# Performance work log

Measured on AMD Instinct MI355X. Metric: run time of the kernel, lower is better.

Reference implementation:

```python
import jax, jax.numpy as jnp
import numpy as np

NUM_HEADS = 16


def setup_inputs() -> dict:
    key = jax.random.key(0)
    ks = jax.random.split(key, 8)
    B, L, Hd = 2, 2048, 1024
    s = 0.02
    return {
        "x": jax.random.normal(ks[0], (B, L, Hd), jnp.float32),
        "y": jax.random.normal(ks[1], (B, L, Hd), jnp.float32),
        "mask": jnp.zeros((B, L), jnp.bool_),  # True = padding (masked out)
        "Wq_w": jax.random.normal(ks[2], (Hd, Hd), jnp.float32) * s,
        "Wq_b": jnp.zeros((Hd,), jnp.float32),
        "Wkv_w": jax.random.normal(ks[3], (Hd, 2 * Hd), jnp.float32) * s,
        "Wkv_b": jnp.zeros((2 * Hd,), jnp.float32),
        "proj_w": jax.random.normal(ks[4], (Hd, Hd), jnp.float32) * s,
        "proj_b": jnp.zeros((Hd,), jnp.float32),
    }


def reference(x, y, mask, Wq_w, Wq_b, Wkv_w, Wkv_b, proj_w, proj_b):
    B, L, Hd = x.shape
    H = NUM_HEADS
    D = Hd // H
    scale = 1.0 / np.sqrt(D)

    # projections (torch Linear: stored here already as (in, out))
    q = (x @ Wq_w + Wq_b).reshape(B, L, H, D).transpose(0, 2, 1, 3)   # bhld
    kv = (y @ Wkv_w + Wkv_b).reshape(B, L, 2, H, D)
    k = kv[:, :, 0].transpose(0, 2, 1, 3)                             # bhkd
    v = kv[:, :, 1].transpose(0, 2, 1, 3)                             # bhkd

    attn = jnp.einsum("bhld,bhkd->bhlk", q, k) * scale

    # combined padding (over keys) + causal mask; True = masked
    causal = jnp.triu(jnp.ones((L, L), jnp.bool_), 1)                 # (L, L)
    combined = mask[:, None, None, :] | causal[None, None]            # (B,1,L,L)
    attn = jnp.where(combined, -jnp.inf, attn)

    p = jax.nn.softmax(attn, axis=-1)
    out = jnp.einsum("bhlk,bhkd->bhld", p, v)
    out = out.transpose(0, 2, 1, 3).reshape(B, L, Hd)
    return out @ proj_w + proj_b
```

## Files before the change

kernel.cpp:

```cpp
#include <hip/hip_runtime.h>
#include <stdint.h>

#define B_  2
#define L_  2048
#define HD_ 1024
#define H_  16
#define D_  64

typedef unsigned short u16;
typedef __attribute__((ext_vector_type(8))) short bf16x8;
typedef __attribute__((ext_vector_type(4))) float f32x4;

#define MFMA16(a, b, c) __builtin_amdgcn_mfma_f32_16x16x32_bf16((a), (b), (c), 0, 0, 0)

__device__ __forceinline__ void gload16(const void* g, void* l) {
  __builtin_amdgcn_global_load_lds((const __attribute__((address_space(1))) void*)g,
                                   (__attribute__((address_space(3))) void*)l, 16, 0, 0);
}

__device__ __forceinline__ u16 f2bf(float f) {
  union { float f; uint32_t u; } c; c.f = f;
  uint32_t u = c.u + 0x7FFFu + ((c.u >> 16) & 1u);
  return (u16)(u >> 16);
}

__device__ __forceinline__ uint32_t cvt_pk_bf16(float lo, float hi) {
  uint32_t r;
  asm("v_cvt_pk_bf16_f32 %0, %1, %2" : "=v"(r) : "v"(lo), "v"(hi));
  return r;
}

__global__ void cast2_k(const float* __restrict__ x, const float* __restrict__ y,
                        u16* __restrict__ xb, u16* __restrict__ yb) {
  int bid = blockIdx.x;
  const float* in = bid < 2048 ? x : y;
  u16* out = bid < 2048 ? xb : yb;
  int i = ((bid & 2047) * 256 + threadIdx.x) * 8;
  float4 a = *(const float4*)(in + i);
  float4 b = *(const float4*)(in + i + 4);
  bf16x8 r;
  r[0] = (short)f2bf(a.x); r[1] = (short)f2bf(a.y); r[2] = (short)f2bf(a.z); r[3] = (short)f2bf(a.w);
  r[4] = (short)f2bf(b.x); r[5] = (short)f2bf(b.y); r[6] = (short)f2bf(b.z); r[7] = (short)f2bf(b.w);
  *(bf16x8*)(out + i) = r;
}

__global__ void wtrans_k(const float* __restrict__ Wq, const float* __restrict__ Wkv,
                         const float* __restrict__ Wp,
                         u16* __restrict__ Wqt, u16* __restrict__ Wkvt, u16* __restrict__ Wpt) {
  int z = blockIdx.z;
  const float* src = z == 0 ? Wq : (z == 1 ? Wkv : Wp);
  u16* dst = z == 0 ? Wqt : (z == 1 ? Wkvt : Wpt);
  int Nfull = (z == 1) ? 2048 : 1024;
  int nb = blockIdx.x * 32;
  if (nb >= Nfull) return;
  __shared__ float tile[32][33];
  int t = threadIdx.x;
  int tc = t & 31, tr = t >> 5;
  int kb = blockIdx.y * 32;
#pragma unroll
  for (int i = 0; i < 4; i++)
    tile[tr + i * 8][tc] = src[(size_t)(kb + tr + i * 8) * Nfull + nb + tc];
  __syncthreads();
#pragma unroll
  for (int i = 0; i < 4; i++) {
    int nl = tr + i * 8;
    dst[(size_t)(nb + nl) * 1024 + kb + tc] = f2bf(tile[tc][nl]);
  }
}

__device__ __forceinline__ void gemm_body(
    char* sA, char* sB,
    const u16* __restrict__ A, const u16* __restrict__ Bt,
    const float* __restrict__ bias, void* __restrict__ outp,
    int N, int epi, int bm, int bn)
{
  int t = threadIdx.x;
  int lane = t & 63, w = t >> 6;
  int g = lane >> 4, l15 = lane & 15;
  int wr = w >> 1, wc = w & 1;

  f32x4 zero = {0.f, 0.f, 0.f, 0.f};
  f32x4 acc[4][4];
#pragma unroll
  for (int mi = 0; mi < 4; mi++)
#pragma unroll
    for (int ni = 0; ni < 4; ni++) acc[mi][ni] = zero;

#define GSTAGE(bufi, k0s) do {                                                          \
    _Pragma("unroll")                                                                   \
    for (int it = 0; it < 4; it++) {                                                    \
      int c = it * 256 + t;                          \
      int r = c >> 3, sp = c & 7;                                                       \
      int off = (sp ^ (r & 7)) << 4;               \
      gload16((const char*)(A + (size_t)(bm + r) * 1024 + (k0s)) + off,                 \
              sA + (bufi) * 16384 + c * 16);                                            \
      gload16((const char*)(Bt + (size_t)(bn + r) * 1024 + (k0s)) + off,                \
              sB + (bufi) * 16384 + c * 16);                                            \
    } } while (0)

  GSTAGE(0, 0);
  int buf = 0;
#pragma unroll 1
  for (int kt = 0; kt < 16; kt++) {
    __builtin_amdgcn_sched_barrier(0);
    __builtin_amdgcn_s_barrier();
    if (kt < 15) {
      GSTAGE(buf ^ 1, (kt + 1) << 6);
      asm volatile("s_waitcnt vmcnt(8)" ::: "memory");
    } else {
      asm volatile("s_waitcnt vmcnt(0)" ::: "memory");
    }
    __builtin_amdgcn_s_barrier();
    __builtin_amdgcn_sched_barrier(0);

    const char* cA = sA + buf * 16384;
    const char* cB = sB + buf * 16384;
#pragma unroll
    for (int kc = 0; kc < 2; kc++) {
      bf16x8 af[4], bfr[4];
#pragma unroll
      for (int mi = 0; mi < 4; mi++) {
        int r = wr * 64 + mi * 16 + l15;
        af[mi] = *(const bf16x8*)(cA + r * 128 + (((kc * 4 + g) ^ (r & 7)) << 4));
      }
#pragma unroll
      for (int ni = 0; ni < 4; ni++) {
        int r = wc * 64 + ni * 16 + l15;
        bfr[ni] = *(const bf16x8*)(cB + r * 128 + (((kc * 4 + g) ^ (r & 7)) << 4));
      }
#pragma unroll
      for (int mi = 0; mi < 4; mi++)
#pragma unroll
        for (int ni = 0; ni < 4; ni++)
          acc[mi][ni] = MFMA16(af[mi], bfr[ni], acc[mi][ni]);
    }
    buf ^= 1;
  }
#undef GSTAGE

  float bv[4];
#pragma unroll
  for (int ni = 0; ni < 4; ni++) bv[ni] = bias[bn + wc * 64 + ni * 16 + l15];

  if (epi == 2) {
    float* fo = (float*)outp;
#pragma unroll
    for (int mi = 0; mi < 4; mi++)
#pragma unroll
      for (int ni = 0; ni < 4; ni++) {
        int n = bn + wc * 64 + ni * 16 + l15;
#pragma unroll
        for (int r = 0; r < 4; r++) {
          int m = bm + wr * 64 + mi * 16 + g * 4 + r;
          fo[(size_t)m * N + n] = acc[mi][ni][r] + bv[ni];
        }
      }
  } else {
    u16* ob = (u16*)outp;
#pragma unroll
    for (int mi = 0; mi < 4; mi++)
#pragma unroll
      for (int ni = 0; ni < 4; ni++) {
        int n = bn + wc * 64 + ni * 16 + l15;
        int kv = n >> 10;
        int hh = (n >> 6) & 15;
        int dd = n & 63;
        int m0 = bm + wr * 64 + mi * 16 + g * 4;
        int bb = m0 >> 11, lq0 = m0 & 2047;
        if (epi == 1 && kv == 1) {
          ushort4 pk;
          pk.x = f2bf(acc[mi][ni][0] + bv[ni]);
          pk.y = f2bf(acc[mi][ni][1] + bv[ni]);
          pk.z = f2bf(acc[mi][ni][2] + bv[ni]);
          pk.w = f2bf(acc[mi][ni][3] + bv[ni]);
          size_t idx = (size_t)(B_ * H_ * L_ * D_) +
                       (((size_t)(bb * H_ + hh) * D_ + dd) * L_ + lq0);
          *(ushort4*)(ob + idx) = pk;
        } else {
#pragma unroll
          for (int r = 0; r < 4; r++) {
            size_t idx = (((size_t)(bb * H_ + hh) * L_ + lq0 + r) * D_) + dd;
            ob[idx] = f2bf(acc[mi][ni][r] + bv[ni]);
          }
        }
      }
  }
}

__global__ __launch_bounds__(256) void qkv_k(
    const u16* __restrict__ xb, const u16* __restrict__ yb,
    const u16* __restrict__ Wqt, const u16* __restrict__ Wkvt,
    const float* __restrict__ Wq_b, const float* __restrict__ Wkv_b,
    u16* __restrict__ Qout, u16* __restrict__ KVout)
{
  __shared__ char sA[2 * 16384];
  __shared__ char sB[2 * 16384];
  int bx = blockIdx.x, by = blockIdx.y;
  if (by < 16) {
    gemm_body(sA, sB, yb, Wkvt, Wkv_b, (void*)KVout, 2048, 1, by * 128, bx * 128);
    __syncthreads();
    gemm_body(sA, sB, yb, Wkvt, Wkv_b, (void*)KVout, 2048, 1, (by + 16) * 128, bx * 128);
  } else {
    gemm_body(sA, sB, xb, Wqt, Wq_b, (void*)Qout, 1024, 0,
              (2 * (by - 16) + (bx >> 3)) * 128, (bx & 7) * 128);
  }
}

__global__ __launch_bounds__(256) void gemm_k(
    const u16* __restrict__ A, const u16* __restrict__ Bt,
    const float* __restrict__ bias, void* __restrict__ outp, int N)
{
  __shared__ char sA[2 * 16384];
  __shared__ char sB[2 * 16384];
  gemm_body(sA, sB, A, Bt, bias, outp, N, 2, blockIdx.y * 128, blockIdx.x * 128);
}

__global__ __launch_bounds__(512, 2) void attn_k(
    const u16* __restrict__ Qb, const u16* __restrict__ Kb, const u16* __restrict__ Vt,
    const unsigned char* __restrict__ pad, u16* __restrict__ Ob)
{
  __shared__ char sK[3][8192];
  __shared__ char sV[3][8192];
  __shared__ char sP[8][2048];
  int t = threadIdx.x, lane = t & 63, w = t >> 6, g = lane >> 4, l15 = lane & 15;
  int x = blockIdx.x, h = blockIdx.y, b = blockIdx.z, bh = b * H_ + h;
  int qb = b ? x : 15 - x;

  const u16* Kbh = Kb + (size_t)bh * L_ * D_;
  const u16* Vbh = Vt + (size_t)bh * D_ * L_;
  const unsigned char* pdb = pad + b * L_;
  const float SCL = 0.125f * 1.44269504089f;
  int psw = l15 & 7;

  int srr = t >> 3, ssp = t & 7;
  int sso = (ssp ^ (srr & 7)) << 4;
#define STAGE(bufi, kt0s) do {                                                        \
    gload16((const char*)(Kbh + (size_t)((kt0s) + srr) * D_) + sso, sK[bufi] + t * 16); \
    gload16((const char*)(Vbh + (size_t)srr * L_ + (kt0s)) + sso, sV[bufi] + t * 16);   \
  } while (0)

  int qw0 = qb * 128 + w * 16;
  int bound = qw0 + 15;
  int nkt = 2 * qb + 2;

  const u16* qp = Qb + ((size_t)bh * L_ + qw0 + l15) * D_ + g * 8;
  bf16x8 qf0 = *(const bf16x8*)qp;
  bf16x8 qf1 = *(const bf16x8*)(qp + 32);

  f32x4 zero = {0.f, 0.f, 0.f, 0.f};
  f32x4 oacc[4];
#pragma unroll
  for (int db = 0; db < 4; db++) oacc[db] = zero;
  float mrun = -1e30f, lrun = 0.f;

  STAGE(0, 0);
  int cb = 0, nb = 1;

#pragma unroll 1
  for (int kt = 0; kt < nkt; kt++) {
    int kt0 = kt << 6;
    __builtin_amdgcn_sched_barrier(0);
    if (kt + 1 < nkt) {
      STAGE(nb, (kt + 1) << 6);
      asm volatile("s_waitcnt vmcnt(2)" ::: "memory");
    } else {
      asm volatile("s_waitcnt vmcnt(0)" ::: "memory");
    }
    __builtin_amdgcn_s_barrier();
    __builtin_amdgcn_sched_barrier(0);

    if (kt0 <= bound) {
      float sc[4][4];
#pragma unroll
      for (int s = 0; s < 4; s++) {
        int kb = kt0 + s * 16;
        bool live = (kb <= bound);
        f32x4 st = zero;
        uint32_t pb = 0;
        if (live) {
          int R = s * 16 + l15, sw = l15 & 7;
          bf16x8 kf0 = *(const bf16x8*)(sK[cb] + R * 128 + ((g ^ sw) << 4));
          bf16x8 kf1 = *(const bf16x8*)(sK[cb] + R * 128 + (((4 + g) ^ sw) << 4));
          st = MFMA16(kf0, qf0, st);
          st = MFMA16(kf1, qf1, st);
          pb = *(const uint32_t*)(pdb + kb + 4 * g);
        }
        bool needm = !live || (kb + 15 > qw0) || (__ballot(pb != 0) != 0);
        if (needm) {
#pragma unroll
          for (int r = 0; r < 4; r++) {
            int key = kb + 4 * g + r;
            bool pm = (pb >> (8 * r)) & 0xffu;
            bool msk = !live || pm || (key > qw0 + l15);
            sc[s][r] = msk ? -1e30f : st[r] * SCL;
          }
        } else {
#pragma unroll
          for (int r = 0; r < 4; r++) sc[s][r] = st[r] * SCL;
        }
      }

      float m0 = fmaxf(fmaxf(sc[0][0], sc[0][1]), fmaxf(sc[0][2], sc[0][3]));
      float m1 = fmaxf(fmaxf(sc[1][0], sc[1][1]), fmaxf(sc[1][2], sc[1][3]));
      float m2 = fmaxf(fmaxf(sc[2][0], sc[2][1]), fmaxf(sc[2][2], sc[2][3]));
      float m3 = fmaxf(fmaxf(sc[3][0], sc[3][1]), fmaxf(sc[3][2], sc[3][3]));
      float mt = fmaxf(fmaxf(m0, m1), fmaxf(m2, m3));
      mt = fmaxf(mt, __shfl_xor(mt, 16));
      mt = fmaxf(mt, __shfl_xor(mt, 32));
      if (!__all(mt <= mrun)) {
        float mnew = fmaxf(mrun, mt);
        float al = __builtin_amdgcn_exp2f(mrun - mnew);
        mrun = mnew;
        lrun *= al;
#pragma unroll
        for (int db = 0; db < 4; db++)
#pragma unroll
          for (int r = 0; r < 4; r++) oacc[db][r] *= al;
      }
      float rs = 0.f;
      char* pwb = sP[w] + l15 * 128 + (g & 1) * 8;
#pragma unroll
      for (int s = 0; s < 4; s++) {
        float p0 = __builtin_amdgcn_exp2f(sc[s][0] - mrun);
        float p1 = __builtin_amdgcn_exp2f(sc[s][1] - mrun);
        float p2 = __builtin_amdgcn_exp2f(sc[s][2] - mrun);
        float p3 = __builtin_amdgcn_exp2f(sc[s][3] - mrun);
        rs += (p0 + p1) + (p2 + p3);
        uint32_t w0 = cvt_pk_bf16(p0, p1), w1 = cvt_pk_bf16(p2, p3);
        char* dst = pwb + (((2 * s + (g >> 1)) ^ psw) << 4);
        *(uint32_t*)dst = w0;
        *(uint32_t*)(dst + 4) = w1;
      }
      rs += __shfl_xor(rs, 16);
      rs += __shfl_xor(rs, 32);
      lrun += rs;

#pragma unroll
      for (int kc = 0; kc < 2; kc++) {
        if (kt0 + 32 * kc <= bound) {
          bf16x8 pf = *(const bf16x8*)(sP[w] + l15 * 128 + (((4 * kc + g) ^ psw) << 4));
#pragma unroll
          for (int db = 0; db < 4; db++) {
            int dR = db * 16 + l15;
            bf16x8 vf = *(const bf16x8*)(sV[cb] + dR * 128 +
                                         (((4 * kc + g) ^ (dR & 7)) << 4));
            oacc[db] = MFMA16(vf, pf, oacc[db]);
          }
        }
      }
    }
    cb = (cb == 2) ? 0 : cb + 1;
    nb = (nb == 2) ? 0 : nb + 1;
  }

  float rl = 1.0f / lrun;
  int q = qw0 + l15;
  u16* op = Ob + ((size_t)b * L_ + q) * HD_ + h * D_ + g * 4;
#pragma unroll
  for (int db = 0; db < 4; db++) {
    ushort4 pk;
    pk.x = f2bf(oacc[db][0] * rl);
    pk.y = f2bf(oacc[db][1] * rl);
    pk.z = f2bf(oacc[db][2] * rl);
    pk.w = f2bf(oacc[db][3] * rl);
    *(ushort4*)(op + db * 16) = pk;
  }
#undef STAGE
}

extern "C" void kernel_launch(void* const* d_in, const int* in_sizes, int n_in,
                              void* d_out, int out_size, void* d_ws, size_t ws_size,
                              hipStream_t stream) {
  const float* x      = (const float*)d_in[0];
  const float* y      = (const float*)d_in[1];
  const unsigned char* mask = (const unsigned char*)d_in[2];
  const float* Wq_w   = (const float*)d_in[3];
  const float* Wq_b   = (const float*)d_in[4];
  const float* Wkv_w  = (const float*)d_in[5];
  const float* Wkv_b  = (const float*)d_in[6];
  const float* proj_w = (const float*)d_in[7];
  const float* proj_b = (const float*)d_in[8];

  char* ws = (char*)d_ws;
  u16* xb   = (u16*)(ws);
  u16* yb   = (u16*)(ws + (size_t)(8  << 20));
  u16* Wqt  = (u16*)(ws + (size_t)(16 << 20));
  u16* Wkvt = (u16*)(ws + (size_t)(18 << 20));
  u16* Wpt  = (u16*)(ws + (size_t)(22 << 20));
  u16* Qb   = (u16*)(ws + (size_t)(24 << 20));
  u16* Kb   = (u16*)(ws + (size_t)(32 << 20));
  u16* Vtb  = (u16*)(ws + (size_t)(40 << 20));
  u16* Ob   = xb;

  hipLaunchKernelGGL(cast2_k, dim3(4096), dim3(256), 0, stream, x, y, xb, yb);
  hipLaunchKernelGGL(wtrans_k, dim3(64, 32, 3), dim3(256), 0, stream,
                     Wq_w, Wkv_w, proj_w, Wqt, Wkvt, Wpt);
  hipLaunchKernelGGL(qkv_k, dim3(16, 32), dim3(256), 0, stream,
                     xb, yb, Wqt, Wkvt, Wq_b, Wkv_b, Qb, Kb);
  hipLaunchKernelGGL(attn_k, dim3(16, H_, B_), dim3(512), 0, stream, Qb, Kb, Vtb, mask, Ob);
  hipLaunchKernelGGL(gemm_k, dim3(8, 32), dim3(256), 0, stream, Ob, Wpt, proj_b, d_out, 1024);
}
```

Measured before the change: 134.2 us.

## Merge cast and weight-transpose kernels; raise wave priority around attention MFMAs

Combines the activation bf16 cast kernel and the weight transpose/cast kernel into one launch with a flat 8192-block grid, and drops the idle blocks the old 3D transpose grid wasted on the smaller weights. It also wraps the QK and PV MFMA sequences in the attention kernel with s_setprio so waves issuing matrix ops get scheduling priority over others. The aim is to save one launch gap and to interleave MFMA issue better across waves. The priority hint may do nothing or may hurt overlap of loads and softmax.

```diff
diff --git a/kernel.cpp b/kernel.cpp
--- a/kernel.cpp
+++ b/kernel.cpp
@@ -30,33 +30,34 @@
   return r;
 }
 
-__global__ void cast2_k(const float* __restrict__ x, const float* __restrict__ y,
-                        u16* __restrict__ xb, u16* __restrict__ yb) {
+__global__ void prologue_k(const float* __restrict__ x, const float* __restrict__ y,
+                           u16* __restrict__ xb, u16* __restrict__ yb,
+                           const float* __restrict__ Wq, const float* __restrict__ Wkv,
+                           const float* __restrict__ Wp,
+                           u16* __restrict__ Wqt, u16* __restrict__ Wkvt,
+                           u16* __restrict__ Wpt) {
   int bid = blockIdx.x;
-  const float* in = bid < 2048 ? x : y;
-  u16* out = bid < 2048 ? xb : yb;
-  int i = ((bid & 2047) * 256 + threadIdx.x) * 8;
-  float4 a = *(const float4*)(in + i);
-  float4 b = *(const float4*)(in + i + 4);
-  bf16x8 r;
-  r[0] = (short)f2bf(a.x); r[1] = (short)f2bf(a.y); r[2] = (short)f2bf(a.z); r[3] = (short)f2bf(a.w);
-  r[4] = (short)f2bf(b.x); r[5] = (short)f2bf(b.y); r[6] = (short)f2bf(b.z); r[7] = (short)f2bf(b.w);
-  *(bf16x8*)(out + i) = r;
-}
-
-__global__ void wtrans_k(const float* __restrict__ Wq, const float* __restrict__ Wkv,
-                         const float* __restrict__ Wp,
-                         u16* __restrict__ Wqt, u16* __restrict__ Wkvt, u16* __restrict__ Wpt) {
-  int z = blockIdx.z;
-  const float* src = z == 0 ? Wq : (z == 1 ? Wkv : Wp);
-  u16* dst = z == 0 ? Wqt : (z == 1 ? Wkvt : Wpt);
-  int Nfull = (z == 1) ? 2048 : 1024;
-  int nb = blockIdx.x * 32;
-  if (nb >= Nfull) return;
+  int t = threadIdx.x;
+  if (bid < 4096) {
+    const float* in = bid < 2048 ? x : y;
+    u16* out = bid < 2048 ? xb : yb;
+    int i = ((bid & 2047) * 256 + t) * 8;
+    float4 a = *(const float4*)(in + i);
+    float4 b = *(const float4*)(in + i + 4);
+    bf16x8 r;
+    r[0] = (short)f2bf(a.x); r[1] = (short)f2bf(a.y); r[2] = (short)f2bf(a.z); r[3] = (short)f2bf(a.w);
+    r[4] = (short)f2bf(b.x); r[5] = (short)f2bf(b.y); r[6] = (short)f2bf(b.z); r[7] = (short)f2bf(b.w);
+    *(bf16x8*)(out + i) = r;
+    return;
+  }
+  int f = bid - 4096;
+  const float* src; u16* dst; int Nfull, bx, by;
+  if (f < 1024)      { src = Wq;  dst = Wqt;  Nfull = 1024; bx = f & 31;  by = f >> 5; }
+  else if (f < 3072) { int g2 = f - 1024; src = Wkv; dst = Wkvt; Nfull = 2048; bx = g2 & 63; by = g2 >> 6; }
+  else               { int g2 = f - 3072; src = Wp;  dst = Wpt;  Nfull = 1024; bx = g2 & 31; by = g2 >> 5; }
   __shared__ float tile[32][33];
-  int t = threadIdx.x;
   int tc = t & 31, tr = t >> 5;
-  int kb = blockIdx.y * 32;
+  int nb = bx * 32, kb = by * 32;
 #pragma unroll
   for (int i = 0; i < 4; i++)
     tile[tr + i * 8][tc] = src[(size_t)(kb + tr + i * 8) * Nfull + nb + tc];
@@ -281,8 +282,10 @@
           int R = s * 16 + l15, sw = l15 & 7;
           bf16x8 kf0 = *(const bf16x8*)(sK[cb] + R * 128 + ((g ^ sw) << 4));
           bf16x8 kf1 = *(const bf16x8*)(sK[cb] + R * 128 + (((4 + g) ^ sw) << 4));
+          __builtin_amdgcn_s_setprio(1);
           st = MFMA16(kf0, qf0, st);
           st = MFMA16(kf1, qf1, st);
+          __builtin_amdgcn_s_setprio(0);
           pb = *(const uint32_t*)(pdb + kb + 4 * g);
         }
         bool needm = !live || (kb + 15 > qw0) || (__ballot(pb != 0) != 0);
@@ -339,6 +342,7 @@
       for (int kc = 0; kc < 2; kc++) {
         if (kt0 + 32 * kc <= bound) {
           bf16x8 pf = *(const bf16x8*)(sP[w] + l15 * 128 + (((4 * kc + g) ^ psw) << 4));
+          __builtin_amdgcn_s_setprio(1);
 #pragma unroll
           for (int db = 0; db < 4; db++) {
             int dR = db * 16 + l15;
@@ -346,6 +350,7 @@
                                          (((4 * kc + g) ^ (dR & 7)) << 4));
             oacc[db] = MFMA16(vf, pf, oacc[db]);
           }
+          __builtin_amdgcn_s_setprio(0);
         }
       }
     }
@@ -392,9 +397,8 @@
   u16* Vtb  = (u16*)(ws + (size_t)(40 << 20));
   u16* Ob   = xb;
 
-  hipLaunchKernelGGL(cast2_k, dim3(4096), dim3(256), 0, stream, x, y, xb, yb);
-  hipLaunchKernelGGL(wtrans_k, dim3(64, 32, 3), dim3(256), 0, stream,
-                     Wq_w, Wkv_w, proj_w, Wqt, Wkvt, Wpt);
+  hipLaunchKernelGGL(prologue_k, dim3(8192), dim3(256), 0, stream,
+                     x, y, xb, yb, Wq_w, Wkv_w, proj_w, Wqt, Wkvt, Wpt);
   hipLaunchKernelGGL(qkv_k, dim3(16, 32), dim3(256), 0, stream,
                      xb, yb, Wqt, Wkvt, Wq_b, Wkv_b, Qb, Kb);
   hipLaunchKernelGGL(attn_k, dim3(16, H_, B_), dim3(512), 0, stream, Qb, Kb, Vtb, mask, Ob);
```

Result: no change. 134.9 us (+0.5%).
